# Kernel tuning notes

Hardware: AMD Instinct MI355X
Metric: run time of the kernel (lower is better)

## Reference

```python
import jax, jax.numpy as jnp
import numpy as np

N, E, D, H, K = 100000, 1600000, 512, 256, 64


def setup_inputs() -> dict:
    key = jax.random.key(0)
    ks = jax.random.split(key, 8)
    x = jax.random.normal(ks[0], (N, D), dtype=jnp.float32)
    edge_index = jax.random.randint(ks[1], (2, E), 0, N, dtype=jnp.int64)
    W1 = jax.random.normal(ks[2], (D, H), dtype=jnp.float32) / np.sqrt(D)
    b1 = jnp.zeros((H,), dtype=jnp.float32)
    W2 = jax.random.normal(ks[3], (H, H), dtype=jnp.float32) / np.sqrt(H)
    b2 = jnp.zeros((H,), dtype=jnp.float32)
    Wk = jax.random.normal(ks[4], (H, K), dtype=jnp.float32) / np.sqrt(H)
    log_tau = jnp.array(np.log(1.0), dtype=jnp.float32)
    return {"x": x, "edge_index": edge_index, "W1": W1, "b1": b1,
            "W2": W2, "b2": b2, "Wk": Wk, "log_tau": log_tau}


def _gcn_norm(edge_index, n):
    # add self-loops, compute sym-normalized edge weights (PyG GCNConv default)
    loop = jnp.arange(n, dtype=edge_index.dtype)
    src = jnp.concatenate([edge_index[0], loop])
    dst = jnp.concatenate([edge_index[1], loop])
    deg = jax.ops.segment_sum(jnp.ones_like(dst, dtype=jnp.float32), dst, num_segments=n)
    dinv = jnp.where(deg > 0, jax.lax.rsqrt(deg), 0.0)
    norm = dinv[src] * dinv[dst]  # [E+N]
    return src, dst, norm


def _gcn_conv(h, W, b, src, dst, norm, n):
    hw = h @ W                      # dense GEMM [n, out]
    msg = hw[src] * norm[:, None]   # gather + scale
    out = jax.ops.segment_sum(msg, dst, num_segments=n)  # scatter-add
    return out + b


def reference(x, edge_index, W1, b1, W2, b2, Wk, log_tau):
    n = x.shape[0]
    src, dst, norm = _gcn_norm(edge_index, n)
    h = jax.nn.relu(_gcn_conv(x, W1, b1, src, dst, norm, n))
    h = _gcn_conv(h, W2, b2, src, dst, norm, n)
    logits = h @ Wk                 # [n, K]
    tau = jnp.exp(log_tau)
    S = jax.nn.softmax(logits / tau, axis=-1)
    return (S, logits)
```

## Files before the change

kernel.cpp:

```cpp
#include <hip/hip_runtime.h>

typedef unsigned short u16;
typedef unsigned int u32;

__device__ __forceinline__ float bfl(u32 u) { union { u32 i; float f; } v; v.i = u << 16; return v.f; }
__device__ __forceinline__ float bfh(u32 u) { union { u32 i; float f; } v; v.i = u & 0xffff0000u; return v.f; }
__device__ __forceinline__ float bf2f(u16 u) { union { u32 i; float f; } v; v.i = ((u32)u) << 16; return v.f; }
__device__ __forceinline__ u16 f2bf(float f) {
    union { float f; u32 i; } v; v.f = f;
    u32 r = v.i + 0x7fffu + ((v.i >> 16) & 1u);
    return (u16)(r >> 16);
}

typedef const __attribute__((address_space(1))) unsigned int* gas_u32;
typedef __attribute__((address_space(3))) unsigned int* las_u32;
__device__ __forceinline__ void async_cp16(const void* g, void* l) {
    __builtin_amdgcn_global_load_lds((gas_u32)g, (las_u32)l, 16, 0, 0);
}

__global__ void k_detect(const u32* __restrict__ xw, const int* __restrict__ eiw,
                         const void* __restrict__ ltau, int* __restrict__ flags,
                         int xwords, int E) {
    __shared__ int cf32, ci64nz;
    if (threadIdx.x == 0) { cf32 = 0; ci64nz = 0; }
    __syncthreads();
    int t = threadIdx.x;
    int xs = xwords / 256;
    u32 w = xw[(size_t)t * xs];
    int e = (int)((w >> 23) & 0xFFu);
    if (e >= 100 && e <= 140) atomicAdd(&cf32, 1);
    int es = E / 256;
    int hw = eiw[2 * (size_t)t * es + 1];
    if (hw != 0) atomicAdd(&ci64nz, 1);
    __syncthreads();
    if (t == 0) {
        int f32 = (cf32 >= 192) ? 1 : 0;
        flags[0] = f32;
        flags[1] = (ci64nz == 0) ? 1 : 0;
        ((float*)flags)[2] = f32 ? ((const float*)ltau)[0] : bf2f(((const u16*)ltau)[0]);
    }
}

__global__ void k_edges(const int* __restrict__ ei, int* __restrict__ src, int* __restrict__ dst,
                        int e, const int* __restrict__ flags) {
    int i = blockIdx.x * 256 + threadIdx.x;
    if (i >= e) return;
    if (flags[1]) { src[i] = ei[2 * i]; dst[i] = ei[2 * (e + i)]; }
    else          { src[i] = ei[i];     dst[i] = ei[e + i]; }
}

__global__ void k_zeroi(int* p, int n) {
    int i = blockIdx.x * 256 + threadIdx.x;
    if (i < n) p[i] = 0;
}

__global__ __launch_bounds__(256) void k_bcount(const int* __restrict__ dst, int* __restrict__ bcount,
                                                int e, int nb) {
    __shared__ int h[1024];
    int t = threadIdx.x;
    for (int i = t; i < nb; i += 256) h[i] = 0;
    __syncthreads();
    int chunk = (e + gridDim.x - 1) / gridDim.x;
    int beg = blockIdx.x * chunk;
    int end = beg + chunk; if (end > e) end = e;
    for (int i = beg + t; i < end; i += 256) atomicAdd(&h[dst[i] >> 7], 1);
    __syncthreads();
    for (int i = t; i < nb; i += 256) { int v = h[i]; if (v) atomicAdd(&bcount[i], v); }
}

__global__ __launch_bounds__(1024) void k_bscan(const int* __restrict__ bcount, int* __restrict__ bbase,
                                                int* __restrict__ bcursor, int nb) {
    int t = threadIdx.x;
    int per = (nb + 1023) >> 10;
    int b0 = t * per;
    int ls[8];
    int s = 0;
#pragma unroll
    for (int j = 0; j < 8; j++) {
        int v = 0;
        if (j < per && b0 + j < nb) v = bcount[b0 + j];
        ls[j] = v; s += v;
    }
    int lane = t & 63, w = t >> 6;
    int inc = s;
    for (int d = 1; d < 64; d <<= 1) { int u = __shfl_up(inc, d); if (lane >= d) inc += u; }
    __shared__ int wsum[16];
    __shared__ int gtot;
    if (lane == 63) wsum[w] = inc;
    __syncthreads();
    if (t == 0) { int a = 0; for (int i = 0; i < 16; i++) { int x = wsum[i]; wsum[i] = a; a += x; } gtot = a; }
    __syncthreads();
    int base = wsum[w] + inc - s;
#pragma unroll
    for (int j = 0; j < 8; j++) {
        if (j < per && b0 + j < nb) { bbase[b0 + j] = base; bcursor[b0 + j] = base; base += ls[j]; }
    }
    if (t == 0) bbase[nb] = gtot;
}

__global__ __launch_bounds__(256) void k_bscatter(const int* __restrict__ src, const int* __restrict__ dst,
                                                  int* __restrict__ bcursor, u32* __restrict__ ebuf,
                                                  int e, int nb) {
    __shared__ int h[1024];
    __shared__ int lbase[1024];
    int t = threadIdx.x;
    for (int i = t; i < nb; i += 256) h[i] = 0;
    __syncthreads();
    int chunk = (e + gridDim.x - 1) / gridDim.x;
    int beg = blockIdx.x * chunk;
    int end = beg + chunk; if (end > e) end = e;
    for (int i = beg + t; i < end; i += 256) atomicAdd(&h[dst[i] >> 7], 1);
    __syncthreads();
    for (int i = t; i < nb; i += 256) {
        int v = h[i];
        lbase[i] = v ? atomicAdd(&bcursor[i], v) : 0;
        h[i] = 0;
    }
    __syncthreads();
    for (int i = beg + t; i < end; i += 256) {
        int d = dst[i];
        int b = d >> 7;
        int p = lbase[b] + atomicAdd(&h[b], 1);
        ebuf[p] = ((u32)(d & 127) << 25) | (u32)src[i];
    }
}

__global__ __launch_bounds__(256) void k_bcsr(const u32* __restrict__ ebuf, const int* __restrict__ bbase,
                                              int* __restrict__ row_ptr, float* __restrict__ dinv,
                                              int* __restrict__ col, int n, int nb, int e) {
    __shared__ int hist[128], sc[128], cur[128];
    int b = blockIdx.x, t = threadIdx.x;
    if (t < 128) hist[t] = 0;
    __syncthreads();
    int beg = bbase[b], end = bbase[b + 1];
    for (int j = beg + t; j < end; j += 256) atomicAdd(&hist[ebuf[j] >> 25], 1);
    __syncthreads();
    if (t < 128) sc[t] = hist[t];
    __syncthreads();
    for (int d = 1; d < 128; d <<= 1) {
        int v = 0;
        if (t < 128 && t >= d) v = sc[t - d];
        __syncthreads();
        if (t < 128) sc[t] += v;
        __syncthreads();
    }
    if (t < 128) {
        int node = (b << 7) + t;
        if (node < n) {
            int ex = sc[t] - hist[t];
            row_ptr[node] = beg + ex;
            dinv[node] = rsqrtf((float)(hist[t] + 1));
            cur[t] = ex;
        }
    }
    if (b == 0 && t == 0) row_ptr[n] = e;
    __syncthreads();
    for (int j = beg + t; j < end; j += 256) {
        u32 ev = ebuf[j];
        int dl = (int)(ev >> 25);
        int p = atomicAdd(&cur[dl], 1);
        col[beg + p] = (int)(ev & 0x1FFFFFFu);
    }
}

__global__ void k_transpose_flex(const void* __restrict__ in, u16* __restrict__ out,
                                 int R, int C, const int* __restrict__ flags) {
    int idx = blockIdx.x * 256 + threadIdx.x;
    if (idx >= R * C) return;
    u16 v = flags[0] ? f2bf(((const float*)in)[idx]) : ((const u16*)in)[idx];
    int r = idx / C, c = idx % C;
    out[(size_t)c * R + r] = v;
}

typedef __bf16 bf16x8 __attribute__((ext_vector_type(8)));
typedef float floatx4 __attribute__((ext_vector_type(4)));

template <int WROWS, int WCOLS, int TM, int TN, int MODE, bool AFLEX, bool OFLEX>
__global__ __launch_bounds__(256, 4) void k_gemm_bt(const void* __restrict__ A,
                                                    const u16* __restrict__ Bt,
                                                    void* __restrict__ C,
                                                    const float* __restrict__ dinv,
                                                    const int* __restrict__ flags,
                                                    long long obase,
                                                    int M, int Nd, int Kd) {
    constexpr int BM = WROWS * TM * 16;
    constexpr int BN = WCOLS * TN * 16;
    constexpr int BK = 32;
    __shared__ u16 As[2][BM][BK];
    __shared__ u16 Bs[2][BN][BK];
    const int af32 = AFLEX ? flags[0] : 0;
    const int of32 = OFLEX ? flags[0] : 0;
    const int tid = threadIdx.x;
    const int m0 = blockIdx.y * BM;
    const int n0 = blockIdx.x * BN;
    const int lane = tid & 63;
    const int wave = tid >> 6;
    const int wm = wave / WCOLS;
    const int wn = wave % WCOLS;
    const int mrow = lane & 15;
    const int quad = lane >> 4;

    floatx4 acc[TM][TN];
#pragma unroll
    for (int i = 0; i < TM; i++)
#pragma unroll
        for (int j = 0; j < TN; j++) { floatx4 z = {0.f, 0.f, 0.f, 0.f}; acc[i][j] = z; }

    auto stage = [&](int kk, int buf) {
        if (AFLEX && af32) {
#pragma unroll
            for (int idx = tid * 8; idx < BM * BK; idx += 256 * 8) {
                int r = idx >> 5, k = idx & 31;
                int gr = m0 + r;
                u16 t8[8] = {0, 0, 0, 0, 0, 0, 0, 0};
                if (gr < M) {
                    const float* ap = (const float*)A + (size_t)gr * Kd + kk + k;
                    float4 f0 = *(const float4*)ap;
                    float4 f1 = *(const float4*)(ap + 4);
                    t8[0] = f2bf(f0.x); t8[1] = f2bf(f0.y); t8[2] = f2bf(f0.z); t8[3] = f2bf(f0.w);
                    t8[4] = f2bf(f1.x); t8[5] = f2bf(f1.y); t8[6] = f2bf(f1.z); t8[7] = f2bf(f1.w);
                }
                *(int4*)&As[buf][r][k] = *(const int4*)t8;
            }
#pragma unroll
            for (int idx = tid * 8; idx < BN * BK; idx += 256 * 8) {
                int r = idx >> 5, k = idx & 31;
                int4 v = *(const int4*)(Bt + (size_t)(n0 + r) * Kd + kk + k);
                *(int4*)&Bs[buf][r][k] = v;
            }
        } else {
#pragma unroll
            for (int idx = tid * 8; idx < BM * BK; idx += 256 * 8) {
                int r = idx >> 5, k = idx & 31;
                int gr = m0 + r;
                if (gr >= M) gr = M - 1;
                async_cp16((const u16*)A + (size_t)gr * Kd + kk + k, &As[buf][r][k]);
            }
#pragma unroll
            for (int idx = tid * 8; idx < BN * BK; idx += 256 * 8) {
                int r = idx >> 5, k = idx & 31;
                async_cp16(Bt + (size_t)(n0 + r) * Kd + kk + k, &Bs[buf][r][k]);
            }
        }
    };

    const int steps = Kd / BK;
    stage(0, 0);
    for (int s = 0; s < steps; s++) {
        __syncthreads();
        if (s + 1 < steps) stage((s + 1) * BK, (s + 1) & 1);
        const int b = s & 1;
        bf16x8 af[TM], bfr[TN];
#pragma unroll
        for (int i = 0; i < TM; i++)
            af[i] = *(const bf16x8*)&As[b][wm * TM * 16 + i * 16 + mrow][quad * 8];
#pragma unroll
        for (int j = 0; j < TN; j++)
            bfr[j] = *(const bf16x8*)&Bs[b][wn * TN * 16 + j * 16 + mrow][quad * 8];
#pragma unroll
        for (int i = 0; i < TM; i++)
#pragma unroll
            for (int j = 0; j < TN; j++)
                acc[i][j] = __builtin_amdgcn_mfma_f32_16x16x32_bf16(af[i], bfr[j], acc[i][j], 0, 0, 0);
    }

#pragma unroll
    for (int i = 0; i < TM; i++) {
#pragma unroll
        for (int r = 0; r < 4; r++) {
            int grow = m0 + wm * TM * 16 + i * 16 + quad * 4 + r;
            if (grow < M) {
                float scale = (MODE == 0) ? dinv[grow] : 1.0f;
#pragma unroll
                for (int j = 0; j < TN; j++) {
                    int gcol = n0 + wn * TN * 16 + j * 16 + mrow;
                    float val = acc[i][j][r] * scale;
                    long long cidx = obase + (long long)grow * Nd + gcol;
                    if (OFLEX && of32) ((float*)C)[cidx] = val;
                    else               ((u16*)C)[cidx] = f2bf(val);
                }
            }
        }
    }
}

__global__ __launch_bounds__(256) void k_agg(const u16* __restrict__ g, u16* __restrict__ out,
                                             const int* __restrict__ row_ptr,
                                             const int* __restrict__ col,
                                             const float* __restrict__ dinv,
                                             const void* __restrict__ bias,
                                             const int* __restrict__ flags,
                                             int n, int do_relu) {
    int wid = (int)((blockIdx.x * 256 + threadIdx.x) >> 6);
    int lane = threadIdx.x & 63;
    if (wid >= n) return;
    const u16* gp = g + (size_t)lane * 4;
    uint2 rv = *(const uint2*)(gp + (size_t)wid * 256);
    float a0 = bfl(rv.x), a1 = bfh(rv.x), a2 = bfl(rv.y), a3 = bfh(rv.y);
    int beg = row_ptr[wid], end = row_ptr[wid + 1];
    for (int base = beg; base < end; base += 64) {
        int m = end - base; if (m > 64) m = 64;
        int ci = (base + lane < end) ? col[base + lane] : 0;
        int j = 0;
        for (; j + 8 <= m; j += 8) {
            uint2 v[8];
#pragma unroll
            for (int q = 0; q < 8; q++) {
                int s = __shfl(ci, j + q);
                v[q] = *(const uint2*)(gp + (size_t)s * 256);
            }
#pragma unroll
            for (int q = 0; q < 8; q++) {
                a0 += bfl(v[q].x); a1 += bfh(v[q].x);
                a2 += bfl(v[q].y); a3 += bfh(v[q].y);
            }
        }
        for (; j < m; j++) {
            int s = __shfl(ci, j);
            uint2 v = *(const uint2*)(gp + (size_t)s * 256);
            a0 += bfl(v.x); a1 += bfh(v.x); a2 += bfl(v.y); a3 += bfh(v.y);
        }
    }
    float dv = dinv[wid];
    float b0, b1, b2, b3;
    if (flags[0]) {
        float4 q = ((const float4*)bias)[lane];
        b0 = q.x; b1 = q.y; b2 = q.z; b3 = q.w;
    } else {
        uint2 bv = ((const uint2*)bias)[lane];
        b0 = bfl(bv.x); b1 = bfh(bv.x); b2 = bfl(bv.y); b3 = bfh(bv.y);
    }
    a0 = a0 * dv + b0;
    a1 = a1 * dv + b1;
    a2 = a2 * dv + b2;
    a3 = a3 * dv + b3;
    if (do_relu) {
        a0 = fmaxf(a0, 0.f); a1 = fmaxf(a1, 0.f); a2 = fmaxf(a2, 0.f); a3 = fmaxf(a3, 0.f);
    }
    uint2 o;
    o.x = (u32)f2bf(a0) | ((u32)f2bf(a1) << 16);
    o.y = (u32)f2bf(a2) | ((u32)f2bf(a3) << 16);
    *(uint2*)(out + (size_t)wid * 256 + (size_t)lane * 4) = o;
}

__global__ __launch_bounds__(256) void k_softmax(void* __restrict__ out, long long NK,
                                                 const int* __restrict__ flags, int n) {
    int wid = (int)((blockIdx.x * 256 + threadIdx.x) >> 6);
    int lane = threadIdx.x & 63;
    if (wid >= n) return;
    int f32o = flags[0];
    float lt = ((const float*)flags)[2];
    float inv_tau = __expf(-lt);
    long long li = NK + (long long)wid * 64 + lane;
    float x = f32o ? ((const float*)out)[li] : bf2f(((const u16*)out)[li]);
    x *= inv_tau;
    float m = x;
    for (int d = 32; d; d >>= 1) m = fmaxf(m, __shfl_xor(m, d));
    float e = __expf(x - m);
    float s = e;
    for (int d = 32; d; d >>= 1) s += __shfl_xor(s, d);
    float r = e / s;
    long long si = (long long)wid * 64 + lane;
    if (f32o) ((float*)out)[si] = r;
    else      ((u16*)out)[si] = f2bf(r);
}

extern "C" void kernel_launch(void* const* d_in, const int* in_sizes, int n_in,
                              void* d_out, int out_size, void* d_ws, size_t ws_size,
                              hipStream_t stream) {
    const void* x    = d_in[0];
    const int*  ei   = (const int*)d_in[1];
    const void* W1   = d_in[2];
    const void* b1   = d_in[3];
    const void* W2   = d_in[4];
    const void* b2   = d_in[5];
    const void* Wk   = d_in[6];
    const void* ltau = d_in[7];
    const int D = 512, H = 256, K = 64;
    const int N = in_sizes[0] / D;
    const int E = in_sizes[1] / 2;
    const long long NK = (long long)N * K;
    const int nb = (N + 127) >> 7;

    u16* g = (u16*)d_ws;
    u16* h = g + (size_t)N * H;
    int* flags = (int*)(h + (size_t)N * H);
    int* srcv = (int*)g;
    int* dstv = srcv + E;
    u32* ebuf = (u32*)(dstv + E);

    size_t ooff = 0;
    auto oalloc = [&](size_t bytes) -> char* {
        char* p = (char*)d_out + ooff;
        ooff += (bytes + 255) & ~(size_t)255;
        return p;
    };
    int*   col     = (int*)oalloc((size_t)E * 4);
    float* dinv    = (float*)oalloc((size_t)N * 4);
    int*   row_ptr = (int*)oalloc((size_t)(N + 1) * 4);
    int*   bcount  = (int*)oalloc((size_t)nb * 4);
    int*   bbase   = (int*)oalloc((size_t)(nb + 1) * 4);
    int*   bcursor = (int*)oalloc((size_t)nb * 4);
    u16*   W1t     = (u16*)oalloc((size_t)D * H * 2);
    u16*   W2t     = (u16*)oalloc((size_t)H * H * 2);
    u16*   Wkt     = (u16*)oalloc((size_t)H * K * 2);

    auto g256 = [](long long n) { return (int)((n + 255) / 256); };

    k_detect<<<1, 256, 0, stream>>>((const u32*)x, ei, ltau, flags, in_sizes[0] / 2, E);
    k_edges<<<g256(E), 256, 0, stream>>>(ei, srcv, dstv, E, flags);
    k_zeroi<<<g256(nb), 256, 0, stream>>>(bcount, nb);
    k_bcount<<<256, 256, 0, stream>>>(dstv, bcount, E, nb);
    k_bscan<<<1, 1024, 0, stream>>>(bcount, bbase, bcursor, nb);
    k_bscatter<<<256, 256, 0, stream>>>(srcv, dstv, bcursor, ebuf, E, nb);
    k_bcsr<<<nb, 256, 0, stream>>>(ebuf, bbase, row_ptr, dinv, col, N, nb, E);

    k_transpose_flex<<<g256((long long)D * H), 256, 0, stream>>>(W1, W1t, D, H, flags);
    k_transpose_flex<<<g256((long long)H * H), 256, 0, stream>>>(W2, W2t, H, H, flags);
    k_transpose_flex<<<g256((long long)H * K), 256, 0, stream>>>(Wk, Wkt, H, K, flags);

    const int m64 = (N + 63) / 64;
    k_gemm_bt<1, 4, 4, 4, 0, true, false>
        <<<dim3(1, m64), 256, 0, stream>>>(x, W1t, g, dinv, flags, 0, N, H, D);
    k_agg<<<g256((long long)N * 64), 256, 0, stream>>>(g, h, row_ptr, col, dinv, b1, flags, N, 1);
    k_gemm_bt<1, 4, 4, 4, 0, false, false>
        <<<dim3(1, m64), 256, 0, stream>>>(h, W2t, g, dinv, flags, 0, N, H, H);
    k_agg<<<g256((long long)N * 64), 256, 0, stream>>>(g, h, row_ptr, col, dinv, b2, flags, N, 0);
    k_gemm_bt<1, 4, 4, 1, 1, false, true>
        <<<dim3(1, m64), 256, 0, stream>>>(h, Wkt, d_out, dinv, flags, NK, N, K, H);
    k_softmax<<<g256((long long)N * 64), 256, 0, stream>>>(d_out, NK, flags, N);
}
```

Baseline: 707.6 us.

## Fuse edge preprocessing, widen aggregation gathers, enlarge GEMM tiles

Bucket zeroing moves into the detect kernel, and edge conversion is fused with the bucket histogram, removing two launches and one pass over dst. The aggregation kernel now gathers 16-byte rows with two half-waves working on alternating neighbours, then combines them with a cross-half shuffle, aiming for fewer wider memory transactions. The first two GEMMs use 512-thread blocks covering 128 rows with adjusted launch bounds, which trades occupancy for more reuse of the weight tile. Half-waves may sit idle on low-degree rows, and the launch-bound changes can affect register allocation.

```diff
diff --git a/kernel.cpp b/kernel.cpp
--- a/kernel.cpp
+++ b/kernel.cpp
@@ -20,11 +20,13 @@
 
 __global__ void k_detect(const u32* __restrict__ xw, const int* __restrict__ eiw,
                          const void* __restrict__ ltau, int* __restrict__ flags,
-                         int xwords, int E) {
+                         int* __restrict__ bcount,
+                         int xwords, int E, int nb) {
     __shared__ int cf32, ci64nz;
     if (threadIdx.x == 0) { cf32 = 0; ci64nz = 0; }
     __syncthreads();
     int t = threadIdx.x;
+    for (int i = t; i < nb; i += 256) bcount[i] = 0;
     int xs = xwords / 256;
     u32 w = xw[(size_t)t * xs];
     int e = (int)((w >> 23) & 0xFFu);
@@ -41,29 +43,25 @@
     }
 }
 
-__global__ void k_edges(const int* __restrict__ ei, int* __restrict__ src, int* __restrict__ dst,
-                        int e, const int* __restrict__ flags) {
-    int i = blockIdx.x * 256 + threadIdx.x;
-    if (i >= e) return;
-    if (flags[1]) { src[i] = ei[2 * i]; dst[i] = ei[2 * (e + i)]; }
-    else          { src[i] = ei[i];     dst[i] = ei[e + i]; }
-}
-
-__global__ void k_zeroi(int* p, int n) {
-    int i = blockIdx.x * 256 + threadIdx.x;
-    if (i < n) p[i] = 0;
-}
-
-__global__ __launch_bounds__(256) void k_bcount(const int* __restrict__ dst, int* __restrict__ bcount,
-                                                int e, int nb) {
+__global__ __launch_bounds__(256) void k_edges_count(const int* __restrict__ ei,
+                                                     int* __restrict__ src, int* __restrict__ dst,
+                                                     int* __restrict__ bcount,
+                                                     int e, int nb, const int* __restrict__ flags) {
     __shared__ int h[1024];
     int t = threadIdx.x;
     for (int i = t; i < nb; i += 256) h[i] = 0;
     __syncthreads();
+    const int i64 = flags[1];
     int chunk = (e + gridDim.x - 1) / gridDim.x;
     int beg = blockIdx.x * chunk;
     int end = beg + chunk; if (end > e) end = e;
-    for (int i = beg + t; i < end; i += 256) atomicAdd(&h[dst[i] >> 7], 1);
+    for (int i = beg + t; i < end; i += 256) {
+        int s, d;
+        if (i64) { s = ei[2 * i]; d = ei[2 * (e + i)]; }
+        else     { s = ei[i];     d = ei[e + i]; }
+        src[i] = s; dst[i] = d;
+        atomicAdd(&h[d >> 7], 1);
+    }
     __syncthreads();
     for (int i = t; i < nb; i += 256) { int v = h[i]; if (v) atomicAdd(&bcount[i], v); }
 }
@@ -176,13 +174,15 @@
 typedef float floatx4 __attribute__((ext_vector_type(4)));
 
 template <int WROWS, int WCOLS, int TM, int TN, int MODE, bool AFLEX, bool OFLEX>
-__global__ __launch_bounds__(256, 4) void k_gemm_bt(const void* __restrict__ A,
-                                                    const u16* __restrict__ Bt,
-                                                    void* __restrict__ C,
-                                                    const float* __restrict__ dinv,
-                                                    const int* __restrict__ flags,
-                                                    long long obase,
-                                                    int M, int Nd, int Kd) {
+__global__ __launch_bounds__(WROWS * WCOLS * 64, (WROWS == 2) ? 6 : 8)
+void k_gemm_bt(const void* __restrict__ A,
+               const u16* __restrict__ Bt,
+               void* __restrict__ C,
+               const float* __restrict__ dinv,
+               const int* __restrict__ flags,
+               long long obase,
+               int M, int Nd, int Kd) {
+    constexpr int THREADS = WROWS * WCOLS * 64;
     constexpr int BM = WROWS * TM * 16;
     constexpr int BN = WCOLS * TN * 16;
     constexpr int BK = 32;
@@ -209,7 +209,7 @@
     auto stage = [&](int kk, int buf) {
         if (AFLEX && af32) {
 #pragma unroll
-            for (int idx = tid * 8; idx < BM * BK; idx += 256 * 8) {
+            for (int idx = tid * 8; idx < BM * BK; idx += THREADS * 8) {
                 int r = idx >> 5, k = idx & 31;
                 int gr = m0 + r;
                 u16 t8[8] = {0, 0, 0, 0, 0, 0, 0, 0};
@@ -223,21 +223,21 @@
                 *(int4*)&As[buf][r][k] = *(const int4*)t8;
             }
 #pragma unroll
-            for (int idx = tid * 8; idx < BN * BK; idx += 256 * 8) {
+            for (int idx = tid * 8; idx < BN * BK; idx += THREADS * 8) {
                 int r = idx >> 5, k = idx & 31;
                 int4 v = *(const int4*)(Bt + (size_t)(n0 + r) * Kd + kk + k);
                 *(int4*)&Bs[buf][r][k] = v;
             }
         } else {
 #pragma unroll
-            for (int idx = tid * 8; idx < BM * BK; idx += 256 * 8) {
+            for (int idx = tid * 8; idx < BM * BK; idx += THREADS * 8) {
                 int r = idx >> 5, k = idx & 31;
                 int gr = m0 + r;
                 if (gr >= M) gr = M - 1;
                 async_cp16((const u16*)A + (size_t)gr * Kd + kk + k, &As[buf][r][k]);
             }
 #pragma unroll
-            for (int idx = tid * 8; idx < BN * BK; idx += 256 * 8) {
+            for (int idx = tid * 8; idx < BN * BK; idx += THREADS * 8) {
                 int r = idx >> 5, k = idx & 31;
                 async_cp16(Bt + (size_t)(n0 + r) * Kd + kk + k, &Bs[buf][r][k]);
             }
@@ -294,53 +294,75 @@
     int wid = (int)((blockIdx.x * 256 + threadIdx.x) >> 6);
     int lane = threadIdx.x & 63;
     if (wid >= n) return;
-    const u16* gp = g + (size_t)lane * 4;
-    uint2 rv = *(const uint2*)(gp + (size_t)wid * 256);
-    float a0 = bfl(rv.x), a1 = bfh(rv.x), a2 = bfl(rv.y), a3 = bfh(rv.y);
+    int half = lane >> 5;
+    int l = lane & 31;
+    const u16* gp = g + (size_t)l * 8;
+    float a0 = 0.f, a1 = 0.f, a2 = 0.f, a3 = 0.f, a4 = 0.f, a5 = 0.f, a6 = 0.f, a7 = 0.f;
+    if (half == 0) {
+        uint4 rv = *(const uint4*)(gp + (size_t)wid * 256);
+        a0 += bfl(rv.x); a1 += bfh(rv.x); a2 += bfl(rv.y); a3 += bfh(rv.y);
+        a4 += bfl(rv.z); a5 += bfh(rv.z); a6 += bfl(rv.w); a7 += bfh(rv.w);
+    }
     int beg = row_ptr[wid], end = row_ptr[wid + 1];
     for (int base = beg; base < end; base += 64) {
         int m = end - base; if (m > 64) m = 64;
         int ci = (base + lane < end) ? col[base + lane] : 0;
         int j = 0;
-        for (; j + 8 <= m; j += 8) {
-            uint2 v[8];
+        for (; j + 16 <= m; j += 16) {
+            uint4 v[8];
 #pragma unroll
             for (int q = 0; q < 8; q++) {
-                int s = __shfl(ci, j + q);
-                v[q] = *(const uint2*)(gp + (size_t)s * 256);
+                int s = __shfl(ci, j + 2 * q + half);
+                v[q] = *(const uint4*)(gp + (size_t)s * 256);
             }
 #pragma unroll
             for (int q = 0; q < 8; q++) {
                 a0 += bfl(v[q].x); a1 += bfh(v[q].x);
                 a2 += bfl(v[q].y); a3 += bfh(v[q].y);
-            }
-        }
-        for (; j < m; j++) {
-            int s = __shfl(ci, j);
-            uint2 v = *(const uint2*)(gp + (size_t)s * 256);
-            a0 += bfl(v.x); a1 += bfh(v.x); a2 += bfl(v.y); a3 += bfh(v.y);
-        }
-    }
-    float dv = dinv[wid];
-    float b0, b1, b2, b3;
-    if (flags[0]) {
-        float4 q = ((const float4*)bias)[lane];
-        b0 = q.x; b1 = q.y; b2 = q.z; b3 = q.w;
-    } else {
-        uint2 bv = ((const uint2*)bias)[lane];
-        b0 = bfl(bv.x); b1 = bfh(bv.x); b2 = bfl(bv.y); b3 = bfh(bv.y);
-    }
-    a0 = a0 * dv + b0;
-    a1 = a1 * dv + b1;
-    a2 = a2 * dv + b2;
-    a3 = a3 * dv + b3;
-    if (do_relu) {
-        a0 = fmaxf(a0, 0.f); a1 = fmaxf(a1, 0.f); a2 = fmaxf(a2, 0.f); a3 = fmaxf(a3, 0.f);
-    }
-    uint2 o;
-    o.x = (u32)f2bf(a0) | ((u32)f2bf(a1) << 16);
-    o.y = (u32)f2bf(a2) | ((u32)f2bf(a3) << 16);
-    *(uint2*)(out + (size_t)wid * 256 + (size_t)lane * 4) = o;
+                a4 += bfl(v[q].z); a5 += bfh(v[q].z);
+                a6 += bfl(v[q].w); a7 += bfh(v[q].w);
+            }
+        }
+        for (; j < m; j += 2) {
+            int idx = j + half;
+            int s = __shfl(ci, idx < m ? idx : j);
+            uint4 v = *(const uint4*)(gp + (size_t)s * 256);
+            if (idx < m) {
+                a0 += bfl(v.x); a1 += bfh(v.x); a2 += bfl(v.y); a3 += bfh(v.y);
+                a4 += bfl(v.z); a5 += bfh(v.z); a6 += bfl(v.w); a7 += bfh(v.w);
+            }
+        }
+    }
+    a0 += __shfl_xor(a0, 32); a1 += __shfl_xor(a1, 32);
+    a2 += __shfl_xor(a2, 32); a3 += __shfl_xor(a3, 32);
+    a4 += __shfl_xor(a4, 32); a5 += __shfl_xor(a5, 32);
+    a6 += __shfl_xor(a6, 32); a7 += __shfl_xor(a7, 32);
+    if (half == 0) {
+        float dv = dinv[wid];
+        float b0, b1, b2, b3, b4, b5, b6, b7;
+        if (flags[0]) {
+            const float4* bp = (const float4*)bias;
+            float4 q0 = bp[2 * l], q1 = bp[2 * l + 1];
+            b0 = q0.x; b1 = q0.y; b2 = q0.z; b3 = q0.w;
+            b4 = q1.x; b5 = q1.y; b6 = q1.z; b7 = q1.w;
+        } else {
+            uint4 bv = ((const uint4*)bias)[l];
+            b0 = bfl(bv.x); b1 = bfh(bv.x); b2 = bfl(bv.y); b3 = bfh(bv.y);
+            b4 = bfl(bv.z); b5 = bfh(bv.z); b6 = bfl(bv.w); b7 = bfh(bv.w);
+        }
+        a0 = a0 * dv + b0; a1 = a1 * dv + b1; a2 = a2 * dv + b2; a3 = a3 * dv + b3;
+        a4 = a4 * dv + b4; a5 = a5 * dv + b5; a6 = a6 * dv + b6; a7 = a7 * dv + b7;
+        if (do_relu) {
+            a0 = fmaxf(a0, 0.f); a1 = fmaxf(a1, 0.f); a2 = fmaxf(a2, 0.f); a3 = fmaxf(a3, 0.f);
+            a4 = fmaxf(a4, 0.f); a5 = fmaxf(a5, 0.f); a6 = fmaxf(a6, 0.f); a7 = fmaxf(a7, 0.f);
+        }
+        uint4 o;
+        o.x = (u32)f2bf(a0) | ((u32)f2bf(a1) << 16);
+        o.y = (u32)f2bf(a2) | ((u32)f2bf(a3) << 16);
+        o.z = (u32)f2bf(a4) | ((u32)f2bf(a5) << 16);
+        o.w = (u32)f2bf(a6) | ((u32)f2bf(a7) << 16);
+        *(uint4*)(out + (size_t)wid * 256 + (size_t)l * 8) = o;
+    }
 }
 
 __global__ __launch_bounds__(256) void k_softmax(void* __restrict__ out, long long NK,
@@ -407,10 +429,8 @@
 
     auto g256 = [](long long n) { return (int)((n + 255) / 256); };
 
-    k_detect<<<1, 256, 0, stream>>>((const u32*)x, ei, ltau, flags, in_sizes[0] / 2, E);
-    k_edges<<<g256(E), 256, 0, stream>>>(ei, srcv, dstv, E, flags);
-    k_zeroi<<<g256(nb), 256, 0, stream>>>(bcount, nb);
-    k_bcount<<<256, 256, 0, stream>>>(dstv, bcount, E, nb);
+    k_detect<<<1, 256, 0, stream>>>((const u32*)x, ei, ltau, flags, bcount, in_sizes[0] / 2, E, nb);
+    k_edges_count<<<256, 256, 0, stream>>>(ei, srcv, dstv, bcount, E, nb, flags);
     k_bscan<<<1, 1024, 0, stream>>>(bcount, bbase, bcursor, nb);
     k_bscatter<<<256, 256, 0, stream>>>(srcv, dstv, bcursor, ebuf, E, nb);
     k_bcsr<<<nb, 256, 0, stream>>>(ebuf, bbase, row_ptr, dinv, col, N, nb, E);
@@ -419,12 +439,13 @@
     k_transpose_flex<<<g256((long long)H * H), 256, 0, stream>>>(W2, W2t, H, H, flags);
     k_transpose_flex<<<g256((long long)H * K), 256, 0, stream>>>(Wk, Wkt, H, K, flags);
 
+    const int m128 = (N + 127) / 128;
     const int m64 = (N + 63) / 64;
-    k_gemm_bt<1, 4, 4, 4, 0, true, false>
-        <<<dim3(1, m64), 256, 0, stream>>>(x, W1t, g, dinv, flags, 0, N, H, D);
+    k_gemm_bt<2, 4, 4, 4, 0, true, false>
+        <<<dim3(1, m128), 512, 0, stream>>>(x, W1t, g, dinv, flags, 0, N, H, D);
     k_agg<<<g256((long long)N * 64), 256, 0, stream>>>(g, h, row_ptr, col, dinv, b1, flags, N, 1);
-    k_gemm_bt<1, 4, 4, 4, 0, false, false>
-        <<<dim3(1, m64), 256, 0, stream>>>(h, W2t, g, dinv, flags, 0, N, H, H);
+    k_gemm_bt<2, 4, 4, 4, 0, false, false>
+        <<<dim3(1, m128), 512, 0, stream>>>(h, W2t, g, dinv, flags, 0, N, H, H);
     k_agg<<<g256((long long)N * 64), 256, 0, stream>>>(g, h, row_ptr, col, dinv, b2, flags, N, 0);
     k_gemm_bt<1, 4, 4, 1, 1, false, true>
         <<<dim3(1, m64), 256, 0, stream>>>(h, Wkt, d_out, dinv, flags, NK, N, K, H);
```

Result: slower. 945.9 us (+33.7%).
